# Kernel optimization log

Measured on AMD Instinct MI355X. Metric: run time of the kernel, lower is better.

The kernel has to match this reference:

```python
import jax, jax.numpy as jnp
import numpy as np

HOP = jnp.array([0, 1, 4, 7, 2, 5, 8, 3, 6, 9, 11, 14, 10, 12, 15, 13, 16])
GRAPH = jnp.array([0, 1, 4, 7, 2, 5, 8, 3, 6, 9, 12, 10, 13, 15, 11, 14, 16])
D_MODEL, L, D_INNER, D_STATE, DT_RANK = 512, 17, 1024, 4, 32


def layernorm(x, w, b, eps=1e-5):
    mu = x.mean(-1, keepdims=True)
    var = ((x - mu) ** 2).mean(-1, keepdims=True)
    return (x - mu) * jax.lax.rsqrt(var + eps) * w + b


def setup_inputs() -> dict:
    key = jax.random.key(0)
    ks = jax.random.split(key, 9)
    B = 4096
    s = lambda k, shape: jax.random.normal(k, shape, jnp.float32) * 0.02
    # A_log init per mamba_ssm: log(1..d_state) repeated over d_inner
    A_log = jnp.log(jnp.broadcast_to(jnp.arange(1, D_STATE + 1, dtype=jnp.float32), (D_INNER, D_STATE)))
    return {
        "x": jax.random.normal(ks[0], (B, L, D_MODEL), jnp.float32),
        "bp_embed": s(ks[1], (1, 5, D_MODEL)),
        "ln_w": jnp.ones((D_MODEL,), jnp.float32),
        "ln_b": jnp.zeros((D_MODEL,), jnp.float32),
        "in_proj_w": s(ks[2], (2 * D_INNER, D_MODEL)),
        "conv_w": 1.0 + s(ks[3], (D_INNER,)),  # d_conv=1 depthwise conv == per-channel scale
        "conv_b": jnp.zeros((D_INNER,), jnp.float32),
        "x_proj_w": s(ks[4], (DT_RANK + 2 * D_STATE, D_INNER)),
        "dt_proj_w": s(ks[5], (D_INNER, DT_RANK)),
        "dt_proj_b": s(ks[6], (D_INNER,)) - 4.0,  # softplus-inverse-ish small dt init
        "A_log": A_log,
        "D": jnp.ones((D_INNER,), jnp.float32),
        "out_proj_w": s(ks[7], (D_MODEL, D_INNER)),
    }


def mamba(u, in_proj_w, conv_w, conv_b, x_proj_w, dt_proj_w, dt_proj_b, A_log, D, out_proj_w):
    # u: [B, L, d_model]
    xz = jnp.einsum('bld,ed->ble', u, in_proj_w)          # [B,L,2*d_inner]
    xm, z = jnp.split(xz, 2, axis=-1)
    xm = jax.nn.silu(xm * conv_w + conv_b)                 # d_conv=1 -> pointwise
    x_dbl = jnp.einsum('ble,fe->blf', xm, x_proj_w)        # [B,L,dt_rank+2*d_state]
    dt_r = x_dbl[..., :DT_RANK]
    Bm = x_dbl[..., DT_RANK:DT_RANK + D_STATE]
    Cm = x_dbl[..., DT_RANK + D_STATE:]
    dt = jax.nn.softplus(jnp.einsum('blr,er->ble', dt_r, dt_proj_w) + dt_proj_b)  # [B,L,d_inner]
    A = -jnp.exp(A_log)                                    # [d_inner,d_state]

    def step(h, inp):
        dt_t, B_t, C_t, x_t = inp                          # [B,di],[B,ds],[B,ds],[B,di]
        dA = jnp.exp(dt_t[..., None] * A)                  # [B,di,ds]
        h = dA * h + (dt_t * x_t)[..., None] * B_t[:, None, :]
        y = jnp.einsum('bes,bs->be', h, C_t)
        return h, y

    bsz = u.shape[0]
    h0 = jnp.zeros((bsz, D_INNER, D_STATE), u.dtype)
    seq = (dt.transpose(1, 0, 2), Bm.transpose(1, 0, 2), Cm.transpose(1, 0, 2), xm.transpose(1, 0, 2))
    _, ys = jax.lax.scan(step, h0, seq)                    # ys: [L,B,d_inner]
    y = ys.transpose(1, 0, 2) + xm * D
    y = y * jax.nn.silu(z)
    return jnp.einsum('ble,de->bld', y, out_proj_w)


def reference(x, bp_embed, ln_w, ln_b, in_proj_w, conv_w, conv_b, x_proj_w,
              dt_proj_w, dt_proj_b, A_log, D, out_proj_w):
    bp = bp_embed
    x_bpe = jnp.concatenate([bp[:, :3], bp[:, :3], bp[:, :3], bp[:, :1],
                             bp[:, 3:], bp[:, :1], bp[:, 3:], bp[:, 3:]], axis=1)  # [1,17,dim]
    x_ssm = x[:, HOP, :] + x_bpe
    x_ssm = layernorm(x_ssm, ln_w, ln_b)
    x_ssm = mamba(x_ssm, in_proj_w, conv_w, conv_b, x_proj_w,
                  dt_proj_w, dt_proj_b, A_log, D, out_proj_w)
    return x + x_ssm[:, GRAPH, :]
```

## Files before the change

### kernel.cpp

```cpp
#include <hip/hip_runtime.h>

typedef unsigned short u16;
typedef unsigned int   u32;
typedef __bf16 bf16_t;
typedef bf16_t bf16x8 __attribute__((ext_vector_type(8)));
typedef float  f32x4  __attribute__((ext_vector_type(4)));

#define DEV static __device__ __forceinline__

__constant__ int c_HOP[17] = {0,1,4,7,2,5,8,3,6,9,11,14,10,12,15,13,16};
__constant__ int c_BPE[17] = {0,1,2,0,1,2,0,1,2,0,3,4,0,3,4,3,4};

DEV u16 f2bf(float f){
  u32 x = __builtin_bit_cast(u32, f);
  x += 0x7fffu + ((x >> 16) & 1u);
  return (u16)(x >> 16);
}
DEV float bf2f(u32 u){ return __builtin_bit_cast(float, u << 16); }
DEV float silu_f(float v){ return v / (1.f + __expf(-v)); }
DEV float softplus_f(float s){ return (s > 20.f) ? s : log1pf(__expf(s)); }

DEV void gll16(const void* g, void* l){
  __builtin_amdgcn_global_load_lds((__attribute__((address_space(1))) void*)g,
                                   (__attribute__((address_space(3))) void*)l,
                                   16, 0, 0);
}

__global__ __launch_bounds__(256) void cvt4(
    const float* __restrict__ s0, u16* __restrict__ d0, int n0,
    const float* __restrict__ s1, u16* __restrict__ d1, int n1,
    const float* __restrict__ s2, u16* __restrict__ d2, int n2,
    const float* __restrict__ s3, u16* __restrict__ d3, int n3)
{
  int t = blockIdx.x * 256 + threadIdx.x;
  if (t < n0){ d0[t] = f2bf(s0[t]); return; }
  t -= n0; if (t < n1){ d1[t] = f2bf(s1[t]); return; }
  t -= n1; if (t < n2){ d2[t] = f2bf(s2[t]); return; }
  t -= n2; if (t < n3){ d3[t] = f2bf(s3[t]); }
}

__global__ __launch_bounds__(256) void ln_gather(
    const float* __restrict__ x, const float* __restrict__ bpe,
    const float* __restrict__ lnw, const float* __restrict__ lnb,
    u16* __restrict__ u)
{
  int tok = blockIdx.x;
  int b = tok / 17;
  int l = tok - b * 17;
  const float* xr = x   + ((size_t)b * 17 + c_HOP[l]) * 512;
  const float* br = bpe + (size_t)c_BPE[l] * 512;
  int tid = threadIdx.x;
  int d0 = tid * 2;
  float2 xv = *(const float2*)(xr + d0);
  float2 bv = *(const float2*)(br + d0);
  float v0 = xv.x + bv.x, v1 = xv.y + bv.y;

  __shared__ float red[8];
  float s = v0 + v1;
  #pragma unroll
  for (int o = 32; o; o >>= 1) s += __shfl_xor(s, o);
  if ((tid & 63) == 0) red[tid >> 6] = s;
  __syncthreads();
  float mu = (red[0] + red[1] + red[2] + red[3]) * (1.f / 512.f);
  float a0 = v0 - mu, a1 = v1 - mu;
  float q = a0 * a0 + a1 * a1;
  #pragma unroll
  for (int o = 32; o; o >>= 1) q += __shfl_xor(q, o);
  if ((tid & 63) == 0) red[4 + (tid >> 6)] = q;
  __syncthreads();
  float var = (red[4] + red[5] + red[6] + red[7]) * (1.f / 512.f);
  float rs = rsqrtf(var + 1e-5f);

  u16 o0 = f2bf(a0 * rs * lnw[d0]     + lnb[d0]);
  u16 o1 = f2bf(a1 * rs * lnw[d0 + 1] + lnb[d0 + 1]);
  u32 pack = (u32)o0 | ((u32)o1 << 16);
  *(u32*)(u + (size_t)tok * 512 + d0) = pack;
}

enum { EPI_SPLIT = 0, EPI_XDBL = 1, EPI_OUT = 2 };

template<int EPI>
__global__ __launch_bounds__(256) void gemm_bt(
    const u16* __restrict__ A, int lda,
    const u16* __restrict__ W, int K, int MT,
    u16* __restrict__ ob0, u16* __restrict__ ob1,
    const float* __restrict__ p0, const float* __restrict__ p1,
    const float* __restrict__ xres, float* __restrict__ fout)
{
  __shared__ u16 sA[128 * 32];
  __shared__ u16 sW[128 * 32];
  int nwg = gridDim.x;
  int cpx = nwg >> 3;
  int wg = (blockIdx.x & 7) * cpx + (blockIdx.x >> 3);
  int NT = nwg / MT;
  int nt = wg % NT, mt = wg / NT;
  int brow = mt * 128, bcol = nt * 128;
  int tid = threadIdx.x, lane = tid & 63, wid = tid >> 6;
  int wm = wid >> 1, wn = wid & 1;

  f32x4 acc[4][4] = {};

  int srow = tid >> 2;
  int sch  = tid & 3;

  for (int kt = 0; kt < K; kt += 32) {
    #pragma unroll
    for (int i = 0; i < 2; i++) {
      int r = i * 64 + srow;
      int c = sch ^ ((r >> 1) & 3);
      gll16(A + (size_t)(brow + r) * lda + kt + c * 8,
            (char*)sA + tid * 16 + i * 4096);
    }
    #pragma unroll
    for (int i = 0; i < 2; i++) {
      int r = i * 64 + srow;
      int c = sch ^ ((r >> 1) & 3);
      gll16(W + (size_t)(bcol + r) * K + kt + c * 8,
            (char*)sW + tid * 16 + i * 4096);
    }
    __syncthreads();

    bf16x8 av[4], bv[4];
    #pragma unroll
    for (int mi = 0; mi < 4; mi++) {
      int r = wm * 64 + mi * 16 + (lane & 15);
      int c = (lane >> 4) ^ ((r >> 1) & 3);
      av[mi] = *(const bf16x8*)((const char*)sA + r * 64 + c * 16);
    }
    #pragma unroll
    for (int ni = 0; ni < 4; ni++) {
      int r = wn * 64 + ni * 16 + (lane & 15);
      int c = (lane >> 4) ^ ((r >> 1) & 3);
      bv[ni] = *(const bf16x8*)((const char*)sW + r * 64 + c * 16);
    }
    #pragma unroll
    for (int mi = 0; mi < 4; mi++)
      #pragma unroll
      for (int ni = 0; ni < 4; ni++)
        acc[mi][ni] = __builtin_amdgcn_mfma_f32_16x16x32_bf16(
            av[mi], bv[ni], acc[mi][ni], 0, 0, 0);
    __syncthreads();
  }

  int r4 = (lane >> 4) * 4;
  int cl = lane & 15;
  #pragma unroll
  for (int mi = 0; mi < 4; mi++) {
    int rowb = brow + wm * 64 + mi * 16 + r4;
    #pragma unroll
    for (int ni = 0; ni < 4; ni++) {
      int col = bcol + wn * 64 + ni * 16 + cl;
      if constexpr (EPI == EPI_SPLIT) {
        bool isx = (col < 1024);
        float cw = isx ? p0[col] : 1.f;
        float cb = isx ? p1[col] : 0.f;
        float rv[4];
        #pragma unroll
        for (int rr = 0; rr < 4; rr++)
          rv[rr] = silu_f(acc[mi][ni][rr] * cw + cb);
        #pragma unroll
        for (int rr = 0; rr < 4; rr++) {
          float ov = __shfl_xor(rv[rr], 1);
          if (!(lane & 1)) {
            u32 pk = (u32)f2bf(rv[rr]) | ((u32)f2bf(ov) << 16);
            size_t rowoff = (size_t)(rowb + rr) * 1024;
            if (isx) *(u32*)(ob0 + rowoff + col) = pk;
            else     *(u32*)(ob1 + rowoff + (col - 1024)) = pk;
          }
        }
      } else if constexpr (EPI == EPI_XDBL) {
        if (col < 40) {
          #pragma unroll
          for (int rr = 0; rr < 4; rr++)
            ob0[(size_t)(rowb + rr) * 40 + col] = f2bf(acc[mi][ni][rr]);
        }
      } else {
        #pragma unroll
        for (int rr = 0; rr < 4; rr++) {
          int row = rowb + rr;
          u32 rw = (u32)row;
          u32 b = rw / 17u;
          int gl = (int)(rw - b * 17u);
          size_t oi = ((size_t)b * 17 + c_HOP[gl]) * 512 + col;
          fout[oi] = xres[oi] + acc[mi][ni][rr];
        }
      }
    }
  }
}

__global__ __launch_bounds__(256) void scan2(
    const u16* __restrict__ xm, const u16* __restrict__ zs,
    const u16* __restrict__ xdbl, const u16* __restrict__ wdt,
    const float* __restrict__ bdt, const float* __restrict__ A_log,
    const float* __restrict__ Dp, u16* __restrict__ y)
{
  __shared__ u16 xs[17 * 40];
  __shared__ u16 dt_s[17][264];

  int b = blockIdx.x >> 2;
  int er0 = (blockIdx.x & 3) * 256;
  int tid = threadIdx.x, lane = tid & 63, wid = tid >> 6;
  int l15 = lane & 15, lhi = lane >> 4;
  const size_t base = (size_t)b * 17 * 1024;

  {
    const u32* src = (const u32*)(xdbl + (size_t)b * 680);
    for (int i = tid; i < 340; i += 256) ((u32*)xs)[i] = src[i];
  }
  __syncthreads();

  {
    bf16x8 a0 = *(const bf16x8*)(xs + l15 * 40 + lhi * 8);
    bf16x8 a1 = *(const bf16x8*)(xs + 16 * 40 + lhi * 8);
    #pragma unroll
    for (int nf = 0; nf < 4; nf++) {
      int colc = wid * 64 + nf * 16 + l15;
      int e = er0 + colc;
      bf16x8 bv = *(const bf16x8*)(wdt + (size_t)e * 32 + lhi * 8);
      f32x4 c0 = {}, c1 = {};
      c0 = __builtin_amdgcn_mfma_f32_16x16x32_bf16(a0, bv, c0, 0, 0, 0);
      c1 = __builtin_amdgcn_mfma_f32_16x16x32_bf16(a1, bv, c1, 0, 0, 0);
      float bb = bdt[e];
      #pragma unroll
      for (int rr = 0; rr < 4; rr++) {
        int t = lhi * 4 + rr;
        if (t < 17) dt_s[t][colc] = f2bf(softplus_f(c0[rr] + bb));
      }
      if (lhi == 0) dt_s[16][colc] = f2bf(softplus_f(c1[0] + bb));
    }
  }
  __syncthreads();

  {
    int e = er0 + tid;
    float4 al = *(const float4*)(A_log + (size_t)e * 4);
    float Av0 = -__expf(al.x), Av1 = -__expf(al.y);
    float Av2 = -__expf(al.z), Av3 = -__expf(al.w);
    float Dv = Dp[e];
    const u16* xmb = xm + base + e;
    const u16* zsb = zs + base + e;
    u16* yb = y + base + e;
    float h0 = 0.f, h1 = 0.f, h2 = 0.f, h3 = 0.f;
    #pragma unroll
    for (int t = 0; t < 17; t++) {
      float dtv = bf2f(dt_s[t][tid]);
      float xv = bf2f(xmb[t * 1024]);
      float zv = bf2f(zsb[t * 1024]);
      uint4 raw = *(const uint4*)(xs + t * 40 + 32);
      float B0 = bf2f(raw.x & 0xffffu), B1 = bf2f(raw.x >> 16);
      float B2 = bf2f(raw.y & 0xffffu), B3 = bf2f(raw.y >> 16);
      float C0 = bf2f(raw.z & 0xffffu), C1 = bf2f(raw.z >> 16);
      float C2 = bf2f(raw.w & 0xffffu), C3 = bf2f(raw.w >> 16);
      float dx = dtv * xv;
      h0 = __expf(dtv * Av0) * h0 + dx * B0;
      h1 = __expf(dtv * Av1) * h1 + dx * B1;
      h2 = __expf(dtv * Av2) * h2 + dx * B2;
      h3 = __expf(dtv * Av3) * h3 + dx * B3;
      float yv = h0 * C0 + h1 * C1 + h2 * C2 + h3 * C3;
      yb[t * 1024] = f2bf((yv + xv * Dv) * zv);
    }
  }
}

extern "C" void kernel_launch(void* const* d_in, const int* in_sizes, int n_in,
                              void* d_out, int out_size, void* d_ws, size_t ws_size,
                              hipStream_t stream) {
  const float* x     = (const float*)d_in[0];
  const float* bpe   = (const float*)d_in[1];
  const float* lnw   = (const float*)d_in[2];
  const float* lnb   = (const float*)d_in[3];
  const float* w_in  = (const float*)d_in[4];
  const float* convw = (const float*)d_in[5];
  const float* convb = (const float*)d_in[6];
  const float* w_xp  = (const float*)d_in[7];
  const float* w_dt  = (const float*)d_in[8];
  const float* b_dt  = (const float*)d_in[9];
  const float* A_log = (const float*)d_in[10];
  const float* Dp    = (const float*)d_in[11];
  const float* w_out = (const float*)d_in[12];
  float* out = (float*)d_out;

  u16* ws = (u16*)d_ws;
  u16* wb_in  = ws;
  u16* wb_out = wb_in  + 1048576;
  u16* wb_xp  = wb_out + 524288;
  u16* wb_dt  = wb_xp  + 40960;
  u16* xm     = wb_dt  + 32768;
  u16* zs     = xm     + 71303168;
  u16* xdbl   = zs     + 71303168;
  u16* yv     = xdbl   + 2785280;
  u16* u      = yv;

  const int MT = 544;

  cvt4<<<6432, 256, 0, stream>>>(w_in, wb_in, 1048576, w_out, wb_out, 524288,
                                 w_xp, wb_xp, 40960, w_dt, wb_dt, 32768);

  ln_gather<<<69632, 256, 0, stream>>>(x, bpe, lnw, lnb, u);

  gemm_bt<EPI_SPLIT><<<MT * 16, 256, 0, stream>>>(
      u, 512, wb_in, 512, MT, xm, zs, convw, convb, nullptr, nullptr);

  gemm_bt<EPI_XDBL><<<MT * 1, 256, 0, stream>>>(
      xm, 1024, wb_xp, 1024, MT, xdbl, nullptr, nullptr, nullptr, nullptr, nullptr);

  scan2<<<16384, 256, 0, stream>>>(xm, zs, xdbl, wb_dt, b_dt, A_log, Dp, yv);

  gemm_bt<EPI_OUT><<<MT * 4, 256, 0, stream>>>(
      yv, 1024, wb_out, 1024, MT, nullptr, nullptr, nullptr, nullptr, x, out);
}
```

Before: 913.6 us.

## Double-buffer LDS tiles in GEMM and simplify split epilogue stores

```diff
diff --git a/kernel.cpp b/kernel.cpp
--- a/kernel.cpp
+++ b/kernel.cpp
@@ -87,8 +87,8 @@
     const float* __restrict__ p0, const float* __restrict__ p1,
     const float* __restrict__ xres, float* __restrict__ fout)
 {
-  __shared__ u16 sA[128 * 32];
-  __shared__ u16 sW[128 * 32];
+  __shared__ u16 sA[2][128 * 32];
+  __shared__ u16 sW[2][128 * 32];
   int nwg = gridDim.x;
   int cpx = nwg >> 3;
   int wg = (blockIdx.x & 7) * cpx + (blockIdx.x >> 3);
@@ -103,42 +103,57 @@
   int srow = tid >> 2;
   int sch  = tid & 3;
 
-  for (int kt = 0; kt < K; kt += 32) {
-    #pragma unroll
-    for (int i = 0; i < 2; i++) {
-      int r = i * 64 + srow;
-      int c = sch ^ ((r >> 1) & 3);
-      gll16(A + (size_t)(brow + r) * lda + kt + c * 8,
-            (char*)sA + tid * 16 + i * 4096);
-    }
-    #pragma unroll
-    for (int i = 0; i < 2; i++) {
-      int r = i * 64 + srow;
-      int c = sch ^ ((r >> 1) & 3);
-      gll16(W + (size_t)(bcol + r) * K + kt + c * 8,
-            (char*)sW + tid * 16 + i * 4096);
-    }
-    __syncthreads();
-
+  const u16* gA0 = A + (size_t)(brow + srow)      * lda + (sch ^ ((srow >> 1) & 3)) * 8;
+  const u16* gA1 = A + (size_t)(brow + 64 + srow) * lda + (sch ^ (((64 + srow) >> 1) & 3)) * 8;
+  const u16* gW0 = W + (size_t)(bcol + srow)      * K   + (sch ^ ((srow >> 1) & 3)) * 8;
+  const u16* gW1 = W + (size_t)(bcol + 64 + srow) * K   + (sch ^ (((64 + srow) >> 1) & 3)) * 8;
+
+  auto STAGE = [&](int buf, int kt) {
+    gll16(gA0 + kt, (char*)sA[buf] + tid * 16);
+    gll16(gA1 + kt, (char*)sA[buf] + tid * 16 + 4096);
+    gll16(gW0 + kt, (char*)sW[buf] + tid * 16);
+    gll16(gW1 + kt, (char*)sW[buf] + tid * 16 + 4096);
+  };
+
+  int aoff[4], boff[4];
+  #pragma unroll
+  for (int mi = 0; mi < 4; mi++) {
+    int r = wm * 64 + mi * 16 + (lane & 15);
+    int c = (lane >> 4) ^ ((r >> 1) & 3);
+    aoff[mi] = r * 64 + c * 16;
+  }
+  #pragma unroll
+  for (int ni = 0; ni < 4; ni++) {
+    int r = wn * 64 + ni * 16 + (lane & 15);
+    int c = (lane >> 4) ^ ((r >> 1) & 3);
+    boff[ni] = r * 64 + c * 16;
+  }
+
+  auto COMPUTE = [&](int buf) {
     bf16x8 av[4], bv[4];
     #pragma unroll
-    for (int mi = 0; mi < 4; mi++) {
-      int r = wm * 64 + mi * 16 + (lane & 15);
-      int c = (lane >> 4) ^ ((r >> 1) & 3);
-      av[mi] = *(const bf16x8*)((const char*)sA + r * 64 + c * 16);
-    }
-    #pragma unroll
-    for (int ni = 0; ni < 4; ni++) {
-      int r = wn * 64 + ni * 16 + (lane & 15);
-      int c = (lane >> 4) ^ ((r >> 1) & 3);
-      bv[ni] = *(const bf16x8*)((const char*)sW + r * 64 + c * 16);
-    }
+    for (int mi = 0; mi < 4; mi++)
+      av[mi] = *(const bf16x8*)((const char*)sA[buf] + aoff[mi]);
+    #pragma unroll
+    for (int ni = 0; ni < 4; ni++)
+      bv[ni] = *(const bf16x8*)((const char*)sW[buf] + boff[ni]);
     #pragma unroll
     for (int mi = 0; mi < 4; mi++)
       #pragma unroll
       for (int ni = 0; ni < 4; ni++)
         acc[mi][ni] = __builtin_amdgcn_mfma_f32_16x16x32_bf16(
             av[mi], bv[ni], acc[mi][ni], 0, 0, 0);
+  };
+
+  int nsteps = K >> 5;
+  STAGE(0, 0);
+  __syncthreads();
+  for (int s = 0; s < nsteps; s += 2) {
+    if (s + 1 < nsteps) STAGE(1, (s + 1) << 5);
+    COMPUTE(0);
+    __syncthreads();
+    if (s + 2 < nsteps) STAGE(0, (s + 2) << 5);
+    COMPUTE(1);
     __syncthreads();
   }
 
@@ -154,20 +169,10 @@
         bool isx = (col < 1024);
         float cw = isx ? p0[col] : 1.f;
         float cb = isx ? p1[col] : 0.f;
-        float rv[4];
+        u16* dst = isx ? (ob0 + col) : (ob1 + col - 1024);
         #pragma unroll
         for (int rr = 0; rr < 4; rr++)
-          rv[rr] = silu_f(acc[mi][ni][rr] * cw + cb);
-        #pragma unroll
-        for (int rr = 0; rr < 4; rr++) {
-          float ov = __shfl_xor(rv[rr], 1);
-          if (!(lane & 1)) {
-            u32 pk = (u32)f2bf(rv[rr]) | ((u32)f2bf(ov) << 16);
-            size_t rowoff = (size_t)(rowb + rr) * 1024;
-            if (isx) *(u32*)(ob0 + rowoff + col) = pk;
-            else     *(u32*)(ob1 + rowoff + (col - 1024)) = pk;
-          }
-        }
+          dst[(size_t)(rowb + rr) * 1024] = f2bf(silu_f(acc[mi][ni][rr] * cw + cb));
       } else if constexpr (EPI == EPI_XDBL) {
         if (col < 40) {
           #pragma unroll
```

New measurement: 854.7 us. -6.4%, faster.
